# Kernel optimization log

Hardware: AMD Instinct MI355X
Metric: run time of the kernel (lower is better)

## Reference

```python
import jax, jax.numpy as jnp
import numpy as np

D = 64          # node/edge feature dim
DIN = 3 * D     # concat [src, edge, dst]
N_NODES = 30000
N_EDGES = 480000


def _lin_init(key, fan_in, fan_out):
    return jax.random.normal(key, (fan_in, fan_out), dtype=jnp.float32) / np.sqrt(fan_in)


def setup_inputs() -> dict:
    key = jax.random.key(0)
    ks = jax.random.split(key, 24)
    inp = {
        "node_feat": jax.random.normal(ks[0], (N_NODES, D), dtype=jnp.float32),
        "edge_feat": jax.random.normal(ks[1], (N_EDGES, D), dtype=jnp.float32),
        "src": jax.random.randint(ks[2], (N_EDGES,), 0, N_NODES, dtype=jnp.int32),
        "dst": jax.random.randint(ks[3], (N_EDGES,), 0, N_NODES, dtype=jnp.int32),
    }
    # GatedMLP params for edge update and node update: each has a 'layers' MLP
    # [192->64->64] (SiLU after both layers) and a 'gates' MLP [192->64->64]
    # (SiLU after hidden only, then sigmoid).
    i = 4
    for pref in ("edge", "node"):
        for branch in ("layers", "gates"):
            inp[f"{pref}_{branch}_W0"] = _lin_init(ks[i], DIN, D); i += 1
            inp[f"{pref}_{branch}_b0"] = jnp.zeros((D,), jnp.float32)
            inp[f"{pref}_{branch}_W1"] = _lin_init(ks[i], D, D); i += 1
            inp[f"{pref}_{branch}_b1"] = jnp.zeros((D,), jnp.float32)
    inp["node_out_W"] = _lin_init(ks[i], D, D)  # Linear(64,64,bias=False)
    return inp


def _gated_mlp(x, lW0, lb0, lW1, lb1, gW0, gb0, gW1, gb1):
    silu = jax.nn.silu
    # layers branch: activate hidden + last
    h = silu(silu(x @ lW0 + lb0) @ lW1 + lb1)
    # gates branch: activate hidden only, sigmoid at the end
    g = silu(x @ gW0 + gb0) @ gW1 + gb1
    return h * jax.nn.sigmoid(g)


def reference(node_feat, edge_feat, src, dst,
              edge_layers_W0, edge_layers_b0, edge_layers_W1, edge_layers_b1,
              edge_gates_W0, edge_gates_b0, edge_gates_W1, edge_gates_b1,
              node_layers_W0, node_layers_b0, node_layers_W1, node_layers_b1,
              node_gates_W0, node_gates_b0, node_gates_W1, node_gates_b1,
              node_out_W):
    h_src = node_feat[src]            # [E, D] gather
    h_dst = node_feat[dst]            # [E, D] gather
    # edge update: gated MLP on [src || edge || dst], residual
    e_in = jnp.concatenate([h_src, edge_feat, h_dst], axis=-1)  # [E, 3D]
    e_new = edge_feat + _gated_mlp(e_in, edge_layers_W0, edge_layers_b0,
                                   edge_layers_W1, edge_layers_b1,
                                   edge_gates_W0, edge_gates_b0,
                                   edge_gates_W1, edge_gates_b1)
    # node messages: gated MLP on [src || new_edge || dst]
    m_in = jnp.concatenate([h_src, e_new, h_dst], axis=-1)      # [E, 3D]
    msg = _gated_mlp(m_in, node_layers_W0, node_layers_b0,
                     node_layers_W1, node_layers_b1,
                     node_gates_W0, node_gates_b0,
                     node_gates_W1, node_gates_b1)
    # scatter-sum to destination nodes, output linear, residual
    agg = jax.ops.segment_sum(msg, dst, num_segments=node_feat.shape[0])
    h_new = node_feat + agg @ node_out_W
    return h_new, e_new
```

## Files before the change

kernel.cpp:

```cpp
#include <hip/hip_runtime.h>
#include <hip/hip_bf16.h>
#include <math.h>

typedef __bf16 bf16_t;
typedef __bf16 bf16x8 __attribute__((ext_vector_type(8)));
typedef float  f32x4  __attribute__((ext_vector_type(4)));

#define MFMA16(a,b,c) __builtin_amdgcn_mfma_f32_16x16x32_bf16((a),(b),(c),0,0,0)

namespace {
constexpr int D    = 64;
constexpr int DIN  = 192;
constexpr int NN   = 30000;
constexpr int NE   = 480000;
constexpr int TILE = 128;
constexpr int NTILES = NE / TILE;

constexpr int SW0 = 200;
constexpr int SW1 = 72;
constexpr int SH  = 72;

constexpr int W0T_SZ = 64 * SW0;
constexpr int W1T_SZ = 64 * SW1;

constexpr int LDS_A = 0;
constexpr int LDS_B = 12800;
constexpr int LDS_C = 22016;
constexpr int LDS_TOT = 31232;

constexpr size_t WS_AGG_BYTES = (size_t)NN * D * 4;
constexpr size_t WS_WT_BYTES  = (size_t)(4 * W0T_SZ + 4 * W1T_SZ) * 2;
constexpr size_t WS_FLAG_OFF  = WS_AGG_BYTES + WS_WT_BYTES;
}

__device__ __forceinline__ bf16x8 ldA(const bf16_t* p) {
  return *(const bf16x8*)p;
}
__device__ __forceinline__ bf16x8 ldA(const float* p) {
  const float4* q4 = (const float4*)p;
  const float4 u = q4[0], v = q4[1];
  bf16x8 r;
  r[0] = (bf16_t)u.x; r[1] = (bf16_t)u.y; r[2] = (bf16_t)u.z; r[3] = (bf16_t)u.w;
  r[4] = (bf16_t)v.x; r[5] = (bf16_t)v.y; r[6] = (bf16_t)v.z; r[7] = (bf16_t)v.w;
  return r;
}

__device__ __forceinline__ void stage16(bf16_t* l, const bf16_t* g, int elems, int t) {
  int4* ls = (int4*)l; const int4* gs = (const int4*)g;
  const int n = elems >> 3;
  for (int i = t; i < n; i += 256) ls[i] = gs[i];
}

__device__ __forceinline__ float silu_f(float v) { return v / (1.f + __expf(-v)); }
__device__ __forceinline__ float sigm_f(float v) { return 1.f / (1.f + __expf(-v)); }

template<typename TN, typename TM>
__device__ __forceinline__ void mlp_l0(f32x4 acc[2][4], const bf16_t* __restrict__ w0t,
    const TN* __restrict__ nf, const TM* __restrict__ mid,
    int sA, int sB, int dA, int dB, int midA, int midB, int midStride,
    int m, int q)
{
  const f32x4 z = {0.f, 0.f, 0.f, 0.f};
  #pragma unroll
  for (int mt = 0; mt < 2; ++mt)
    #pragma unroll
    for (int nt = 0; nt < 4; ++nt) acc[mt][nt] = z;
  #pragma unroll
  for (int kt = 0; kt < 6; ++kt) {
    const int ko = (kt & 1) * 32 + q * 8;
    bf16x8 a0, a1;
    if (kt < 2)      { a0 = ldA(nf + sA * D + ko);            a1 = ldA(nf + sB * D + ko); }
    else if (kt < 4) { a0 = ldA(mid + midA * midStride + ko); a1 = ldA(mid + midB * midStride + ko); }
    else             { a0 = ldA(nf + dA * D + ko);            a1 = ldA(nf + dB * D + ko); }
    const bf16_t* wb = w0t + m * SW0 + kt * 32 + q * 8;
    #pragma unroll
    for (int nt = 0; nt < 4; ++nt) {
      const bf16x8 b = ldA(wb + nt * 16 * SW0);
      acc[0][nt] = MFMA16(a0, b, acc[0][nt]);
      acc[1][nt] = MFMA16(a1, b, acc[1][nt]);
    }
  }
}

__device__ __forceinline__ void mlp_l1(f32x4 acc[2][4], const bf16_t* __restrict__ h,
                                       const bf16_t* __restrict__ w1t,
                                       int leA, int leB, int m, int q)
{
  const f32x4 z = {0.f, 0.f, 0.f, 0.f};
  #pragma unroll
  for (int mt = 0; mt < 2; ++mt)
    #pragma unroll
    for (int nt = 0; nt < 4; ++nt) acc[mt][nt] = z;
  #pragma unroll
  for (int kt = 0; kt < 2; ++kt) {
    const int ko = kt * 32 + q * 8;
    const bf16x8 a0 = ldA(h + leA * SH + ko);
    const bf16x8 a1 = ldA(h + leB * SH + ko);
    const bf16_t* wb = w1t + m * SW1 + ko;
    #pragma unroll
    for (int nt = 0; nt < 4; ++nt) {
      const bf16x8 b = ldA(wb + nt * 16 * SW1);
      acc[0][nt] = MFMA16(a0, b, acc[0][nt]);
      acc[1][nt] = MFMA16(a1, b, acc[1][nt]);
    }
  }
}

template<typename TB>
__device__ __forceinline__ void hidden_silu(const f32x4 acc[2][4],
    const TB* __restrict__ bias, bf16_t* __restrict__ h, int w, int m, int q)
{
  #pragma unroll
  for (int nt = 0; nt < 4; ++nt) {
    const float bv = (float)bias[nt * 16 + m];
    #pragma unroll
    for (int mt = 0; mt < 2; ++mt) {
      #pragma unroll
      for (int r = 0; r < 4; ++r) {
        const float v = acc[mt][nt][r] + bv;
        h[(w * 32 + mt * 16 + q * 4 + r) * SH + nt * 16 + m] = (bf16_t)silu_f(v);
      }
    }
  }
}

__global__ void detect_kernel(const void* w0, int* flag) {
  __shared__ int cnt;
  if (threadIdx.x == 0) cnt = 0;
  __syncthreads();
  const unsigned short* u = (const unsigned short*)w0;
  const unsigned short v = u[2 * threadIdx.x];
  const int e = (v >> 7) & 0xFF;
  atomicAdd(&cnt, (e >= 100 && e <= 140) ? 1 : 0);
  __syncthreads();
  if (threadIdx.x == 0) *flag = (cnt >= 128) ? 1 : 0;
}

struct PrepArgs { const void* w[8]; bf16_t* o[8]; };

template<typename T>
__global__ void prep_kernel(const int* flag, int want, PrepArgs a) {
  if (*flag != want) return;
  const int b = blockIdx.x, t = threadIdx.x;
  const T* w = (const T*)a.w[b];
  bf16_t* o = a.o[b];
  if (b < 4) {
    for (int i = t; i < DIN * D; i += 256) o[(i & 63) * SW0 + (i >> 6)] = (bf16_t)(float)w[i];
  } else {
    for (int i = t; i < D * D; i += 256) o[(i & 63) * SW1 + (i >> 6)] = (bf16_t)(float)w[i];
  }
}

template<typename T>
__global__ __launch_bounds__(256, 2) void fused_kernel(
    const int* __restrict__ flag, int want,
    const T* __restrict__ nf, const T* __restrict__ ef,
    const int* __restrict__ src, const int* __restrict__ dst,
    const T* __restrict__ eLb0, const T* __restrict__ eLb1,
    const T* __restrict__ eGb0, const T* __restrict__ eGb1,
    const T* __restrict__ nLb0, const T* __restrict__ nLb1,
    const T* __restrict__ nGb0, const T* __restrict__ nGb1,
    const bf16_t* __restrict__ wt, float* __restrict__ agg,
    T* __restrict__ out_e)
{
  if (*flag != want) return;
  __shared__ __align__(16) bf16_t sm[LDS_TOT];
  const int t = threadIdx.x;
  const int lane = t & 63;
  const int w = t >> 6;
  const int m = lane & 15;
  const int q = lane >> 4;

  const bf16_t* w0t_eL = wt;
  const bf16_t* w0t_eG = wt + W0T_SZ;
  const bf16_t* w0t_nL = wt + 2 * W0T_SZ;
  const bf16_t* w0t_nG = wt + 3 * W0T_SZ;
  const bf16_t* w1t_e  = wt + 4 * W0T_SZ;
  const bf16_t* w1t_n  = wt + 4 * W0T_SZ + 2 * W1T_SZ;

  for (int tile = blockIdx.x; tile < NTILES; tile += gridDim.x) {
    const int e0  = tile * TILE;
    const int eA  = e0 + w * 32 + m;
    const int eB  = eA + 16;
    const int leA = w * 32 + m;
    const int leB = leA + 16;
    const int sA = src[eA], sB = src[eB];
    const int dA = dst[eA], dB = dst[eB];

    f32x4 acc[2][4], acg[2][4];

    stage16(sm + LDS_A, w0t_eL, W0T_SZ, t);
    __syncthreads();
    mlp_l0(acc, sm + LDS_A, nf, ef, sA, sB, dA, dB, eA, eB, D, m, q);
    hidden_silu(acc, eLb0, sm + LDS_B, w, m, q);
    __syncthreads();
    stage16(sm + LDS_A, w0t_eG, W0T_SZ, t);
    __syncthreads();
    mlp_l0(acc, sm + LDS_A, nf, ef, sA, sB, dA, dB, eA, eB, D, m, q);
    hidden_silu(acc, eGb0, sm + LDS_C, w, m, q);
    __syncthreads();
    stage16(sm + LDS_A, w1t_e, 2 * W1T_SZ, t);
    __syncthreads();
    mlp_l1(acc, sm + LDS_B, sm + LDS_A,          leA, leB, m, q);
    mlp_l1(acg, sm + LDS_C, sm + LDS_A + W1T_SZ, leA, leB, m, q);

    bf16_t ev[2][4][4];
    #pragma unroll
    for (int nt = 0; nt < 4; ++nt) {
      const int n = nt * 16 + m;
      const float bL = (float)eLb1[n];
      const float bG = (float)eGb1[n];
      #pragma unroll
      for (int mt = 0; mt < 2; ++mt) {
        #pragma unroll
        for (int r = 0; r < 4; ++r) {
          const int e = e0 + w * 32 + mt * 16 + q * 4 + r;
          const float hv = silu_f(acc[mt][nt][r] + bL);
          const float gv = sigm_f(acg[mt][nt][r] + bG);
          const float val = (float)ef[e * D + n] + hv * gv;
          ev[mt][nt][r] = (bf16_t)val;
          out_e[e * D + n] = (T)val;
        }
      }
    }
    __syncthreads();
    #pragma unroll
    for (int nt = 0; nt < 4; ++nt)
      #pragma unroll
      for (int mt = 0; mt < 2; ++mt)
        #pragma unroll
        for (int r = 0; r < 4; ++r)
          sm[LDS_B + (w * 32 + mt * 16 + q * 4 + r) * SH + nt * 16 + m] = ev[mt][nt][r];
    __syncthreads();

    stage16(sm + LDS_A, w0t_nL, W0T_SZ, t);
    __syncthreads();
    mlp_l0(acc, sm + LDS_A, nf, sm + LDS_B, sA, sB, dA, dB, leA, leB, SH, m, q);
    hidden_silu(acc, nLb0, sm + LDS_C, w, m, q);
    __syncthreads();
    stage16(sm + LDS_A, w0t_nG, W0T_SZ, t);
    __syncthreads();
    mlp_l0(acc, sm + LDS_A, nf, sm + LDS_B, sA, sB, dA, dB, leA, leB, SH, m, q);
    __syncthreads();
    hidden_silu(acc, nGb0, sm + LDS_B, w, m, q);
    __syncthreads();
    stage16(sm + LDS_A, w1t_n, 2 * W1T_SZ, t);
    __syncthreads();
    mlp_l1(acc, sm + LDS_C, sm + LDS_A,          leA, leB, m, q);
    mlp_l1(acg, sm + LDS_B, sm + LDS_A + W1T_SZ, leA, leB, m, q);

    int d8[2][4];
    #pragma unroll
    for (int mt = 0; mt < 2; ++mt)
      #pragma unroll
      for (int r = 0; r < 4; ++r)
        d8[mt][r] = dst[e0 + w * 32 + mt * 16 + q * 4 + r];

    #pragma unroll
    for (int nt = 0; nt < 4; ++nt) {
      const int n = nt * 16 + m;
      const float bL = (float)nLb1[n];
      const float bG = (float)nGb1[n];
      #pragma unroll
      for (int mt = 0; mt < 2; ++mt) {
        #pragma unroll
        for (int r = 0; r < 4; ++r) {
          const float hv = silu_f(acc[mt][nt][r] + bL);
          const float gv = sigm_f(acg[mt][nt][r] + bG);
          atomicAdd(&agg[d8[mt][r] * D + n], hv * gv);
        }
      }
    }
    __syncthreads();
  }
}

template<typename T>
__global__ __launch_bounds__(256) void node_out_kernel(
    const int* __restrict__ flag, int want,
    const T* __restrict__ nf, const float* __restrict__ agg,
    const T* __restrict__ Wo, T* __restrict__ out_h)
{
  if (*flag != want) return;
  __shared__ float wsh[D * D];
  const int t = threadIdx.x;
  for (int i = t; i < D * D; i += 256) wsh[i] = (float)Wo[i];
  __syncthreads();
  const int node = blockIdx.x * 4 + (t >> 6);
  const int j = t & 63;
  const float* arow = agg + node * D;
  float acc = 0.f;
  #pragma unroll
  for (int k = 0; k < D; ++k) acc = fmaf(arow[k], wsh[k * D + j], acc);
  out_h[node * D + j] = (T)((float)nf[node * D + j] + acc);
}

template<typename T>
static void launch_all(void* const* d_in, void* d_out, void* d_ws,
                       const int* flag, int want, bf16_t* wt, float* agg,
                       hipStream_t stream) {
  const T* nf  = (const T*)d_in[0];
  const T* ef  = (const T*)d_in[1];
  const int* src = (const int*)d_in[2];
  const int* dst = (const int*)d_in[3];
  T* out_h = (T*)d_out;
  T* out_e = out_h + (size_t)NN * D;

  fused_kernel<T><<<512, 256, 0, stream>>>(flag, want, nf, ef, src, dst,
      (const T*)d_in[5],  (const T*)d_in[7],
      (const T*)d_in[9],  (const T*)d_in[11],
      (const T*)d_in[13], (const T*)d_in[15],
      (const T*)d_in[17], (const T*)d_in[19],
      wt, agg, out_e);
  node_out_kernel<T><<<NN / 4, 256, 0, stream>>>(flag, want, nf, agg,
      (const T*)d_in[20], out_h);
}

extern "C" void kernel_launch(void* const* d_in, const int* in_sizes, int n_in,
                              void* d_out, int out_size, void* d_ws, size_t ws_size,
                              hipStream_t stream) {
  float*  agg  = (float*)d_ws;
  bf16_t* wt   = (bf16_t*)((char*)d_ws + WS_AGG_BYTES);
  int*    flag = (int*)((char*)d_ws + WS_FLAG_OFF);

  hipMemsetAsync(d_ws, 0, WS_AGG_BYTES, stream);

  detect_kernel<<<1, 256, 0, stream>>>(d_in[4], flag);

  PrepArgs pa;
  pa.w[0] = d_in[4];  pa.w[1] = d_in[8];  pa.w[2] = d_in[12]; pa.w[3] = d_in[16];
  pa.w[4] = d_in[6];  pa.w[5] = d_in[10]; pa.w[6] = d_in[14]; pa.w[7] = d_in[18];
  for (int i = 0; i < 4; ++i) pa.o[i]     = wt + i * W0T_SZ;
  for (int j = 0; j < 4; ++j) pa.o[4 + j] = wt + 4 * W0T_SZ + j * W1T_SZ;
  prep_kernel<float> <<<8, 256, 0, stream>>>(flag, 0, pa);
  prep_kernel<bf16_t><<<8, 256, 0, stream>>>(flag, 1, pa);

  launch_all<float> (d_in, d_out, d_ws, flag, 0, wt, agg, stream);
  launch_all<bf16_t>(d_in, d_out, d_ws, flag, 1, wt, agg, stream);
}
```

Baseline: 613.1 us.

## Keep all W0 weights resident in LDS and process edges per-wave without block syncs

Loads all four layer-0 weight matrices (XOR-swizzled) into LDS once per block instead of re-staging them every tile. Each wave now independently processes 32-edge units with its own scratch buffer, so the per-stage __syncthreads become wave-local lgkmcnt waits. Gate and layer branches share the gathered A fragments held in registers, and W1 is read from global memory into registers. This removes repeated weight staging and block barriers, at the cost of much higher register pressure, a larger LDS footprint and fewer blocks.

```diff
diff --git a/kernel.cpp b/kernel.cpp
--- a/kernel.cpp
+++ b/kernel.cpp
@@ -13,20 +13,20 @@
 constexpr int DIN  = 192;
 constexpr int NN   = 30000;
 constexpr int NE   = 480000;
-constexpr int TILE = 128;
-constexpr int NTILES = NE / TILE;
-
-constexpr int SW0 = 200;
-constexpr int SW1 = 72;
-constexpr int SH  = 72;
-
-constexpr int W0T_SZ = 64 * SW0;
+
+constexpr int NBLK   = 256;
+constexpr int NTHR   = 512;
+constexpr int NUNITS = NE / 32;
+constexpr int NWAVES = NBLK * (NTHR / 64);
+
+constexpr int W0R    = 192;
+constexpr int W0T_SZ = 64 * W0R;
+constexpr int SW1    = 72;
 constexpr int W1T_SZ = 64 * SW1;
-
-constexpr int LDS_A = 0;
-constexpr int LDS_B = 12800;
-constexpr int LDS_C = 22016;
-constexpr int LDS_TOT = 31232;
+constexpr int HBS    = 32 * 64;
+
+constexpr int LDS_SCR = 4 * W0T_SZ;
+constexpr int LDS_TOT = LDS_SCR + 8 * HBS;
 
 constexpr size_t WS_AGG_BYTES = (size_t)NN * D * 4;
 constexpr size_t WS_WT_BYTES  = (size_t)(4 * W0T_SZ + 4 * W1T_SZ) * 2;
@@ -45,80 +45,88 @@
   return r;
 }
 
-__device__ __forceinline__ void stage16(bf16_t* l, const bf16_t* g, int elems, int t) {
-  int4* ls = (int4*)l; const int4* gs = (const int4*)g;
-  const int n = elems >> 3;
-  for (int i = t; i < n; i += 256) ls[i] = gs[i];
-}
-
 __device__ __forceinline__ float silu_f(float v) { return v / (1.f + __expf(-v)); }
 __device__ __forceinline__ float sigm_f(float v) { return 1.f / (1.f + __expf(-v)); }
 
-template<typename TN, typename TM>
-__device__ __forceinline__ void mlp_l0(f32x4 acc[2][4], const bf16_t* __restrict__ w0t,
-    const TN* __restrict__ nf, const TM* __restrict__ mid,
-    int sA, int sB, int dA, int dB, int midA, int midB, int midStride,
-    int m, int q)
+__device__ __forceinline__ void wfence() {
+  __builtin_amdgcn_sched_barrier(0);
+  asm volatile("s_waitcnt lgkmcnt(0)" ::: "memory");
+  __builtin_amdgcn_sched_barrier(0);
+}
+
+__device__ __forceinline__ void mlp_l0m(f32x4 accL[2][4], f32x4 accG[2][4],
+    const bf16_t* __restrict__ w0L, const bf16_t* __restrict__ w0G,
+    const bf16x8 fa[6][2], const int ksw[6], int m)
 {
   const f32x4 z = {0.f, 0.f, 0.f, 0.f};
   #pragma unroll
-  for (int mt = 0; mt < 2; ++mt)
-    #pragma unroll
-    for (int nt = 0; nt < 4; ++nt) acc[mt][nt] = z;
+  for (int h = 0; h < 2; ++h)
+    #pragma unroll
+    for (int nt = 0; nt < 4; ++nt) { accL[h][nt] = z; accG[h][nt] = z; }
+  __builtin_amdgcn_s_setprio(1);
   #pragma unroll
   for (int kt = 0; kt < 6; ++kt) {
-    const int ko = (kt & 1) * 32 + q * 8;
-    bf16x8 a0, a1;
-    if (kt < 2)      { a0 = ldA(nf + sA * D + ko);            a1 = ldA(nf + sB * D + ko); }
-    else if (kt < 4) { a0 = ldA(mid + midA * midStride + ko); a1 = ldA(mid + midB * midStride + ko); }
-    else             { a0 = ldA(nf + dA * D + ko);            a1 = ldA(nf + dB * D + ko); }
-    const bf16_t* wb = w0t + m * SW0 + kt * 32 + q * 8;
+    const bf16_t* pL = w0L + m * W0R + ksw[kt];
+    const bf16_t* pG = w0G + m * W0R + ksw[kt];
     #pragma unroll
     for (int nt = 0; nt < 4; ++nt) {
-      const bf16x8 b = ldA(wb + nt * 16 * SW0);
-      acc[0][nt] = MFMA16(a0, b, acc[0][nt]);
-      acc[1][nt] = MFMA16(a1, b, acc[1][nt]);
-    }
-  }
-}
-
-__device__ __forceinline__ void mlp_l1(f32x4 acc[2][4], const bf16_t* __restrict__ h,
-                                       const bf16_t* __restrict__ w1t,
-                                       int leA, int leB, int m, int q)
+      const bf16x8 bL = *(const bf16x8*)(pL + nt * 16 * W0R);
+      const bf16x8 bG = *(const bf16x8*)(pG + nt * 16 * W0R);
+      accL[0][nt] = MFMA16(fa[kt][0], bL, accL[0][nt]);
+      accL[1][nt] = MFMA16(fa[kt][1], bL, accL[1][nt]);
+      accG[0][nt] = MFMA16(fa[kt][0], bG, accG[0][nt]);
+      accG[1][nt] = MFMA16(fa[kt][1], bG, accG[1][nt]);
+    }
+  }
+  __builtin_amdgcn_s_setprio(0);
+}
+
+__device__ __forceinline__ void loadW1(bf16x8 wb[2][4],
+                                       const bf16_t* __restrict__ w1, int m, int q) {
+  #pragma unroll
+  for (int kt = 0; kt < 2; ++kt)
+    #pragma unroll
+    for (int nt = 0; nt < 4; ++nt)
+      wb[kt][nt] = ldA(w1 + (nt * 16 + m) * SW1 + kt * 32 + q * 8);
+}
+
+__device__ __forceinline__ void mlp_l1r(f32x4 acc[2][4],
+    const bf16_t* __restrict__ hb, const bf16x8 wb[2][4], const int ksw[6], int m)
 {
   const f32x4 z = {0.f, 0.f, 0.f, 0.f};
   #pragma unroll
-  for (int mt = 0; mt < 2; ++mt)
-    #pragma unroll
-    for (int nt = 0; nt < 4; ++nt) acc[mt][nt] = z;
+  for (int h = 0; h < 2; ++h)
+    #pragma unroll
+    for (int nt = 0; nt < 4; ++nt) acc[h][nt] = z;
+  __builtin_amdgcn_s_setprio(1);
   #pragma unroll
   for (int kt = 0; kt < 2; ++kt) {
-    const int ko = kt * 32 + q * 8;
-    const bf16x8 a0 = ldA(h + leA * SH + ko);
-    const bf16x8 a1 = ldA(h + leB * SH + ko);
-    const bf16_t* wb = w1t + m * SW1 + ko;
+    const bf16x8 a0 = *(const bf16x8*)(hb + m * 64 + ksw[kt]);
+    const bf16x8 a1 = *(const bf16x8*)(hb + (m + 16) * 64 + ksw[kt]);
     #pragma unroll
     for (int nt = 0; nt < 4; ++nt) {
-      const bf16x8 b = ldA(wb + nt * 16 * SW1);
-      acc[0][nt] = MFMA16(a0, b, acc[0][nt]);
-      acc[1][nt] = MFMA16(a1, b, acc[1][nt]);
-    }
-  }
+      acc[0][nt] = MFMA16(a0, wb[kt][nt], acc[0][nt]);
+      acc[1][nt] = MFMA16(a1, wb[kt][nt], acc[1][nt]);
+    }
+  }
+  __builtin_amdgcn_s_setprio(0);
 }
 
 template<typename TB>
 __device__ __forceinline__ void hidden_silu(const f32x4 acc[2][4],
-    const TB* __restrict__ bias, bf16_t* __restrict__ h, int w, int m, int q)
+    const TB* __restrict__ bias, bf16_t* __restrict__ hb, int m, int q)
 {
   #pragma unroll
   for (int nt = 0; nt < 4; ++nt) {
     const float bv = (float)bias[nt * 16 + m];
     #pragma unroll
-    for (int mt = 0; mt < 2; ++mt) {
+    for (int h = 0; h < 2; ++h) {
       #pragma unroll
       for (int r = 0; r < 4; ++r) {
-        const float v = acc[mt][nt][r] + bv;
-        h[(w * 32 + mt * 16 + q * 4 + r) * SH + nt * 16 + m] = (bf16_t)silu_f(v);
+        const float v = acc[h][nt][r] + bv;
+        const int row = h * 16 + q * 4 + r;
+        const int col = (nt * 16 + m) ^ (((q * 4 + r) & 7) << 3);
+        hb[row * 64 + col] = (bf16_t)silu_f(v);
       }
     }
   }
@@ -145,14 +153,17 @@
   const T* w = (const T*)a.w[b];
   bf16_t* o = a.o[b];
   if (b < 4) {
-    for (int i = t; i < DIN * D; i += 256) o[(i & 63) * SW0 + (i >> 6)] = (bf16_t)(float)w[i];
+    for (int i = t; i < DIN * D; i += 256) {
+      const int n = i & 63, k = i >> 6;
+      o[(n * W0R + k) ^ ((n & 7) << 3)] = (bf16_t)(float)w[i];
+    }
   } else {
     for (int i = t; i < D * D; i += 256) o[(i & 63) * SW1 + (i >> 6)] = (bf16_t)(float)w[i];
   }
 }
 
 template<typename T>
-__global__ __launch_bounds__(256, 2) void fused_kernel(
+__global__ __launch_bounds__(NTHR, 2) void fused_kernel(
     const int* __restrict__ flag, int want,
     const T* __restrict__ nf, const T* __restrict__ ef,
     const int* __restrict__ src, const int* __restrict__ dst,
@@ -166,95 +177,111 @@
   if (*flag != want) return;
   __shared__ __align__(16) bf16_t sm[LDS_TOT];
   const int t = threadIdx.x;
+
+  {
+    int4* ls = (int4*)sm; const int4* gs = (const int4*)wt;
+    for (int i = t; i < (LDS_SCR >> 3); i += NTHR) ls[i] = gs[i];
+  }
+  __syncthreads();
+
   const int lane = t & 63;
-  const int w = t >> 6;
-  const int m = lane & 15;
-  const int q = lane >> 4;
-
-  const bf16_t* w0t_eL = wt;
-  const bf16_t* w0t_eG = wt + W0T_SZ;
-  const bf16_t* w0t_nL = wt + 2 * W0T_SZ;
-  const bf16_t* w0t_nG = wt + 3 * W0T_SZ;
-  const bf16_t* w1t_e  = wt + 4 * W0T_SZ;
-  const bf16_t* w1t_n  = wt + 4 * W0T_SZ + 2 * W1T_SZ;
-
-  for (int tile = blockIdx.x; tile < NTILES; tile += gridDim.x) {
-    const int e0  = tile * TILE;
-    const int eA  = e0 + w * 32 + m;
-    const int eB  = eA + 16;
-    const int leA = w * 32 + m;
-    const int leB = leA + 16;
+  const int w    = t >> 6;
+  const int m    = lane & 15;
+  const int q    = lane >> 4;
+  bf16_t* hb = sm + LDS_SCR + w * HBS;
+
+  int ksw[6];
+  #pragma unroll
+  for (int kt = 0; kt < 6; ++kt) ksw[kt] = (kt * 32 + q * 8) ^ ((m & 7) << 3);
+
+  const bf16_t* w0eL = sm;
+  const bf16_t* w0eG = sm + W0T_SZ;
+  const bf16_t* w0nL = sm + 2 * W0T_SZ;
+  const bf16_t* w0nG = sm + 3 * W0T_SZ;
+  const bf16_t* w1g  = wt + 4 * W0T_SZ;
+
+  for (int u = blockIdx.x * (NTHR / 64) + w; u < NUNITS; u += NWAVES) {
+    const int e0 = u * 32;
+    const int eA = e0 + m, eB = eA + 16;
     const int sA = src[eA], sB = src[eB];
     const int dA = dst[eA], dB = dst[eB];
 
-    f32x4 acc[2][4], acg[2][4];
-
-    stage16(sm + LDS_A, w0t_eL, W0T_SZ, t);
-    __syncthreads();
-    mlp_l0(acc, sm + LDS_A, nf, ef, sA, sB, dA, dB, eA, eB, D, m, q);
-    hidden_silu(acc, eLb0, sm + LDS_B, w, m, q);
-    __syncthreads();
-    stage16(sm + LDS_A, w0t_eG, W0T_SZ, t);
-    __syncthreads();
-    mlp_l0(acc, sm + LDS_A, nf, ef, sA, sB, dA, dB, eA, eB, D, m, q);
-    hidden_silu(acc, eGb0, sm + LDS_C, w, m, q);
-    __syncthreads();
-    stage16(sm + LDS_A, w1t_e, 2 * W1T_SZ, t);
-    __syncthreads();
-    mlp_l1(acc, sm + LDS_B, sm + LDS_A,          leA, leB, m, q);
-    mlp_l1(acg, sm + LDS_C, sm + LDS_A + W1T_SZ, leA, leB, m, q);
-
-    bf16_t ev[2][4][4];
+    wfence();
+
+    bf16x8 fa[6][2];
+    #pragma unroll
+    for (int kt = 0; kt < 2; ++kt) {
+      const int ko = kt * 32 + q * 8;
+      fa[kt][0]     = ldA(nf + (size_t)sA * D + ko);
+      fa[kt][1]     = ldA(nf + (size_t)sB * D + ko);
+      fa[2 + kt][0] = ldA(ef + (size_t)eA * D + ko);
+      fa[2 + kt][1] = ldA(ef + (size_t)eB * D + ko);
+      fa[4 + kt][0] = ldA(nf + (size_t)dA * D + ko);
+      fa[4 + kt][1] = ldA(nf + (size_t)dB * D + ko);
+    }
+
+    bf16x8 w1L[2][4], w1G[2][4];
+    loadW1(w1L, w1g + 0 * W1T_SZ, m, q);
+    loadW1(w1G, w1g + 1 * W1T_SZ, m, q);
+
+    f32x4 accL[2][4], accG[2][4], hl[2][4], gl[2][4];
+
+    mlp_l0m(accL, accG, w0eL, w0eG, fa, ksw, m);
+    hidden_silu(accL, eLb0, hb, m, q);
+    wfence();
+    mlp_l1r(hl, hb, w1L, ksw, m);
+    wfence();
+    hidden_silu(accG, eGb0, hb, m, q);
+    wfence();
+    mlp_l1r(gl, hb, w1G, ksw, m);
+    wfence();
+
+    loadW1(w1L, w1g + 2 * W1T_SZ, m, q);
+    loadW1(w1G, w1g + 3 * W1T_SZ, m, q);
+
     #pragma unroll
     for (int nt = 0; nt < 4; ++nt) {
       const int n = nt * 16 + m;
       const float bL = (float)eLb1[n];
       const float bG = (float)eGb1[n];
       #pragma unroll
-      for (int mt = 0; mt < 2; ++mt) {
+      for (int h = 0; h < 2; ++h) {
         #pragma unroll
         for (int r = 0; r < 4; ++r) {
-          const int e = e0 + w * 32 + mt * 16 + q * 4 + r;
-          const float hv = silu_f(acc[mt][nt][r] + bL);
-          const float gv = sigm_f(acg[mt][nt][r] + bG);
-          const float val = (float)ef[e * D + n] + hv * gv;
-          ev[mt][nt][r] = (bf16_t)val;
-          out_e[e * D + n] = (T)val;
+          const int e = e0 + h * 16 + q * 4 + r;
+          const float hv = silu_f(hl[h][nt][r] + bL);
+          const float gv = sigm_f(gl[h][nt][r] + bG);
+          const float val = (float)ef[(size_t)e * D + n] + hv * gv;
+          out_e[(size_t)e * D + n] = (T)val;
+          const int row = h * 16 + q * 4 + r;
+          const int col = n ^ (((q * 4 + r) & 7) << 3);
+          hb[row * 64 + col] = (bf16_t)val;
         }
       }
     }
-    __syncthreads();
-    #pragma unroll
-    for (int nt = 0; nt < 4; ++nt)
-      #pragma unroll
-      for (int mt = 0; mt < 2; ++mt)
-        #pragma unroll
-        for (int r = 0; r < 4; ++r)
-          sm[LDS_B + (w * 32 + mt * 16 + q * 4 + r) * SH + nt * 16 + m] = ev[mt][nt][r];
-    __syncthreads();
-
-    stage16(sm + LDS_A, w0t_nL, W0T_SZ, t);
-    __syncthreads();
-    mlp_l0(acc, sm + LDS_A, nf, sm + LDS_B, sA, sB, dA, dB, leA, leB, SH, m, q);
-    hidden_silu(acc, nLb0, sm + LDS_C, w, m, q);
-    __syncthreads();
-    stage16(sm + LDS_A, w0t_nG, W0T_SZ, t);
-    __syncthreads();
-    mlp_l0(acc, sm + LDS_A, nf, sm + LDS_B, sA, sB, dA, dB, leA, leB, SH, m, q);
-    __syncthreads();
-    hidden_silu(acc, nGb0, sm + LDS_B, w, m, q);
-    __syncthreads();
-    stage16(sm + LDS_A, w1t_n, 2 * W1T_SZ, t);
-    __syncthreads();
-    mlp_l1(acc, sm + LDS_C, sm + LDS_A,          leA, leB, m, q);
-    mlp_l1(acg, sm + LDS_B, sm + LDS_A + W1T_SZ, leA, leB, m, q);
+    wfence();
+    #pragma unroll
+    for (int kt = 0; kt < 2; ++kt) {
+      fa[2 + kt][0] = ldA(hb + m * 64 + ksw[kt]);
+      fa[2 + kt][1] = ldA(hb + (m + 16) * 64 + ksw[kt]);
+    }
+    wfence();
+
+    mlp_l0m(accL, accG, w0nL, w0nG, fa, ksw, m);
+    hidden_silu(accL, nLb0, hb, m, q);
+    wfence();
+    mlp_l1r(hl, hb, w1L, ksw, m);
+    wfence();
+    hidden_silu(accG, nGb0, hb, m, q);
+    wfence();
+    mlp_l1r(gl, hb, w1G, ksw, m);
 
     int d8[2][4];
     #pragma unroll
-    for (int mt = 0; mt < 2; ++mt)
+    for (int h = 0; h < 2; ++h)
       #pragma unroll
       for (int r = 0; r < 4; ++r)
-        d8[mt][r] = dst[e0 + w * 32 + mt * 16 + q * 4 + r];
+        d8[h][r] = dst[e0 + h * 16 + q * 4 + r];
 
     #pragma unroll
     for (int nt = 0; nt < 4; ++nt) {
@@ -262,16 +289,15 @@
       const float bL = (float)nLb1[n];
       const float bG = (float)nGb1[n];
       #pragma unroll
-      for (int mt = 0; mt < 2; ++mt) {
+      for (int h = 0; h < 2; ++h) {
         #pragma unroll
         for (int r = 0; r < 4; ++r) {
-          const float hv = silu_f(acc[mt][nt][r] + bL);
-          const float gv = sigm_f(acg[mt][nt][r] + bG);
-          atomicAdd(&agg[d8[mt][r] * D + n], hv * gv);
+          const float hv = silu_f(hl[h][nt][r] + bL);
+          const float gv = sigm_f(gl[h][nt][r] + bG);
+          atomicAdd(&agg[(size_t)d8[h][r] * D + n], hv * gv);
         }
       }
     }
-    __syncthreads();
   }
 }
 
@@ -306,7 +332,7 @@
   T* out_h = (T*)d_out;
   T* out_e = out_h + (size_t)NN * D;
 
-  fused_kernel<T><<<512, 256, 0, stream>>>(flag, want, nf, ef, src, dst,
+  fused_kernel<T><<<NBLK, NTHR, 0, stream>>>(flag, want, nf, ef, src, dst,
       (const T*)d_in[5],  (const T*)d_in[7],
       (const T*)d_in[9],  (const T*)d_in[11],
       (const T*)d_in[13], (const T*)d_in[15],
```

Measured after the change: 647.1 us. 1.06x slower.
